# Kernel tuning notes

Measured on AMD Instinct MI355X. Metric: run time of the kernel, lower is better.

The kernel has to match this reference:

```python
import jax, jax.numpy as jnp
import numpy as np

N_NODES = 50000
N_EDGES = 800000
IN_FEAT = 64
HIDDEN = 32
GRID = 4
OUT = 1
N_GRAPHS = 128
N_CONV = 2  # num_layers - 1
NEG_SLOPE = 0.01  # torch LeakyReLU default


def kan_apply(x, W, bias=None):
    # x: (B, in), W: (2, out, in, grid) -> (B, out)
    g = W.shape[-1]
    k = jnp.arange(1, g + 1, dtype=x.dtype)          # (grid,)
    arg = x[:, :, None] * k                           # (B, in, grid)
    y = (jnp.einsum('big,oig->bo', jnp.cos(arg), W[0])
         + jnp.einsum('big,oig->bo', jnp.sin(arg), W[1]))
    if bias is not None:
        y = y + bias
    return y


def setup_inputs() -> dict:
    key = jax.random.key(0)
    ks = jax.random.split(key, 8)
    x = jax.random.normal(ks[0], (N_NODES, IN_FEAT), dtype=jnp.float32)
    edge_index = jax.random.randint(ks[1], (2, N_EDGES), 0, N_NODES, dtype=jnp.int64)
    batch = jnp.sort(jax.random.randint(ks[2], (N_NODES,), 0, N_GRAPHS, dtype=jnp.int64))
    W_in = jax.random.normal(ks[3], (2, HIDDEN, IN_FEAT, GRID), dtype=jnp.float32) / np.float32(np.sqrt(IN_FEAT) * np.sqrt(GRID))
    W_conv = jax.random.normal(ks[4], (N_CONV, 2, HIDDEN, HIDDEN, GRID), dtype=jnp.float32) / np.float32(np.sqrt(HIDDEN) * np.sqrt(GRID))
    W_out = jax.random.normal(ks[5], (2, OUT, HIDDEN, 1), dtype=jnp.float32) / np.float32(np.sqrt(HIDDEN) * 1.0)
    b_out = jnp.zeros((1, OUT), dtype=jnp.float32)
    return {"x": x, "edge_index": edge_index, "batch": batch,
            "W_in": W_in, "W_conv": W_conv, "W_out": W_out, "b_out": b_out}


def reference(x, edge_index, batch, W_in, W_conv, W_out, b_out):
    # input KAN projection: (N, in_feat) -> (N, hidden)
    h = kan_apply(x, W_in)
    src, dst = edge_index[0], edge_index[1]
    for l in range(N_CONV):
        # message: Fourier-KAN transform of gathered source features (E, hidden)
        m_edge = kan_apply(h[src], W_conv[l])
        # aggregate: scatter-add to destination nodes
        m = jax.ops.segment_sum(m_edge, dst, num_segments=N_NODES)
        h = jax.nn.leaky_relu(m + h, negative_slope=NEG_SLOPE)
    # mean pool per graph
    sums = jax.ops.segment_sum(h, batch, num_segments=N_GRAPHS)
    counts = jax.ops.segment_sum(jnp.ones((h.shape[0], 1), h.dtype), batch, num_segments=N_GRAPHS)
    y = sums / jnp.maximum(counts, 1.0)
    # readout: KAN_linear (grid=1, with bias) + sigmoid
    out = jax.nn.sigmoid(kan_apply(y, W_out, b_out))
    return out
```

## Files before the change

kernel.cpp:

```cpp
#include <hip/hip_runtime.h>
#include <math.h>

#define N_NODES   50000
#define N_EDGES   800000
#define IN_FEAT   64
#define HIDDEN    32
#define GRID_SZ   4
#define N_GRAPHS  128
#define NEG_SLOPE 0.01f
#define SCAN_BLOCKS 196

__global__ __launch_bounds__(256) void zero_int_kernel(int* __restrict__ p, int n) {
  const int i = blockIdx.x * 256 + threadIdx.x;
  if (i < n) p[i] = 0;
}
__global__ __launch_bounds__(256) void zero_kernel(float* __restrict__ p, int n) {
  const int i = blockIdx.x * 256 + threadIdx.x;
  if (i < n) p[i] = 0.f;
}

__global__ __launch_bounds__(256) void hist_kernel(
    const int* __restrict__ dst, int* __restrict__ deg) {
  const int e = blockIdx.x * 256 + threadIdx.x;
  if (e < N_EDGES) atomicAdd(&deg[dst[e]], 1);
}

__global__ __launch_bounds__(256) void scanA_kernel(
    const int* __restrict__ deg, int* __restrict__ bsum) {
  const int i = blockIdx.x * 256 + threadIdx.x;
  int v = (i < N_NODES) ? deg[i] : 0;
#pragma unroll
  for (int o = 32; o > 0; o >>= 1) v += __shfl_down(v, o, 64);
  __shared__ int ws[4];
  if ((threadIdx.x & 63) == 0) ws[threadIdx.x >> 6] = v;
  __syncthreads();
  if (threadIdx.x == 0) bsum[blockIdx.x] = ws[0] + ws[1] + ws[2] + ws[3];
}

__global__ __launch_bounds__(256) void scanB_kernel(
    int* __restrict__ bsum, int* __restrict__ row_ptr) {
  __shared__ int sh[256];
  const int t = threadIdx.x;
  int v = (t < SCAN_BLOCKS) ? bsum[t] : 0;
  sh[t] = v;
  __syncthreads();
  for (int o = 1; o < 256; o <<= 1) {
    const int u = (t >= o) ? sh[t - o] : 0;
    __syncthreads();
    sh[t] += u;
    __syncthreads();
  }
  bsum[t] = (t == 0) ? 0 : sh[t - 1];
  if (t == 0) row_ptr[N_NODES] = N_EDGES;
}

__global__ __launch_bounds__(256) void scanC_kernel(
    const int* __restrict__ deg, const int* __restrict__ bsum,
    int* __restrict__ row_ptr, int* __restrict__ cursor) {
  __shared__ int sh[256];
  const int t = threadIdx.x;
  const int i = blockIdx.x * 256 + t;
  const int v = (i < N_NODES) ? deg[i] : 0;
  sh[t] = v;
  __syncthreads();
  for (int o = 1; o < 256; o <<= 1) {
    const int u = (t >= o) ? sh[t - o] : 0;
    __syncthreads();
    sh[t] += u;
    __syncthreads();
  }
  if (i < N_NODES) {
    const int excl = bsum[blockIdx.x] + sh[t] - v;
    row_ptr[i] = excl;
    cursor[i] = excl;
  }
}

__global__ __launch_bounds__(256) void fill_kernel(
    const int* __restrict__ src, const int* __restrict__ dst,
    int* __restrict__ cursor, int* __restrict__ adj) {
  const int e = blockIdx.x * 256 + threadIdx.x;
  if (e < N_EDGES) {
    const int pos = atomicAdd(&cursor[dst[e]], 1);
    adj[pos] = src[e];
  }
}

__global__ __launch_bounds__(256) void gather_update_v2(
    const float* __restrict__ T, const int* __restrict__ row_ptr,
    const int* __restrict__ adj, float* __restrict__ H) {
  const int gid = blockIdx.x * 256 + threadIdx.x;
  const int n = gid >> 3;
  const int q = gid & 7;
  if (n >= N_NODES) return;
  const int lo = row_ptr[n], hi = row_ptr[n + 1];
  const float4* __restrict__ T4 = reinterpret_cast<const float4*>(T);
  float4 acc = make_float4(0.f, 0.f, 0.f, 0.f);
  for (int k = lo; k < hi; ++k) {
    const int s = adj[k];
    const float4 t = T4[s * 8 + q];
    acc.x += t.x; acc.y += t.y; acc.z += t.z; acc.w += t.w;
  }
  float4* __restrict__ H4 = reinterpret_cast<float4*>(H);
  float4 h = H4[n * 8 + q];
  h.x += acc.x; h.y += acc.y; h.z += acc.z; h.w += acc.w;
  h.x = (h.x >= 0.f) ? h.x : NEG_SLOPE * h.x;
  h.y = (h.y >= 0.f) ? h.y : NEG_SLOPE * h.y;
  h.z = (h.z >= 0.f) ? h.z : NEG_SLOPE * h.z;
  h.w = (h.w >= 0.f) ? h.w : NEG_SLOPE * h.w;
  H4[n * 8 + q] = h;
}

__global__ __launch_bounds__(256, 2) void kan_input_v9(
    const float* __restrict__ X, const float* __restrict__ W,
    float* __restrict__ H) {
  extern __shared__ float smem[];
  float4* __restrict__ w4 = reinterpret_cast<float4*>(smem);
  float* __restrict__ tg = smem + 16384;
  const int tid = threadIdx.x;
  const int n0 = blockIdx.x * 128;

  const float4* __restrict__ Wg = reinterpret_cast<const float4*>(W);
#pragma unroll
  for (int r = 0; r < 16; ++r) {
    const int idx = r * 256 + tid;
    const int part = idx >> 11;
    const int rem = idx & 2047;
    const int o = rem >> 6;
    const int i = rem & 63;
    w4[part * 2048 + o * 64 + (i ^ ((o >> 2) & 7))] = Wg[idx];
  }

  const int oq = tid & 7;
  const int grp = tid >> 3;
  const int nb = 4 * grp;

  float acc[4][4];
#pragma unroll
  for (int n = 0; n < 4; ++n)
#pragma unroll
    for (int q = 0; q < 4; ++q) acc[n][q] = 0.f;

  for (int ch = 0; ch < 8; ++ch) {
    __syncthreads();
#pragma unroll
    for (int p = 0; p < 4; ++p) {
      const int lin = p * 256 + tid;
      const int il = lin & 7;
      const int node = lin >> 3;
      const int gn = n0 + node;
      const int gs = (gn < N_NODES) ? gn : (N_NODES - 1);
      const float v = X[gs * IN_FEAT + ch * 8 + il];
      float s1, c1;
      sincosf(v, &s1, &c1);
      *reinterpret_cast<float2*>(&tg[il * 260 + node * 2]) = make_float2(c1, s1);
    }
    __syncthreads();
#pragma unroll
    for (int il = 0; il < 8; ++il) {
      const int i = ch * 8 + il;
      const float4 tA = *reinterpret_cast<const float4*>(&tg[il * 260 + nb * 2]);
      const float4 tB = *reinterpret_cast<const float4*>(&tg[il * 260 + nb * 2 + 4]);
      const float bc[4] = {tA.x, tA.z, tB.x, tB.z};
      const float bs[4] = {tA.y, tA.w, tB.y, tB.w};
      float cN[4][4], sN[4][4];
#pragma unroll
      for (int n = 0; n < 4; ++n) {
        const float c1 = bc[n], s1 = bs[n];
        const float c2 = c1*c1 - s1*s1, s2 = s1*c1 + c1*s1;
        const float c3 = c2*c1 - s2*s1, s3 = s2*c1 + c2*s1;
        const float c4 = c3*c1 - s3*s1, s4 = s3*c1 + c3*s1;
        cN[n][0]=c1; cN[n][1]=c2; cN[n][2]=c3; cN[n][3]=c4;
        sN[n][0]=s1; sN[n][1]=s2; sN[n][2]=s3; sN[n][3]=s4;
      }
      const int sl = i ^ oq;
#pragma unroll
      for (int q = 0; q < 4; ++q) {
        const float4 a = w4[(4 * oq + q) * 64 + sl];
        const float4 b = w4[2048 + (4 * oq + q) * 64 + sl];
#pragma unroll
        for (int n = 0; n < 4; ++n)
          acc[n][q] += cN[n][0]*a.x + cN[n][1]*a.y + cN[n][2]*a.z + cN[n][3]*a.w
                     + sN[n][0]*b.x + sN[n][1]*b.y + sN[n][2]*b.z + sN[n][3]*b.w;
      }
    }
  }
#pragma unroll
  for (int n = 0; n < 4; ++n) {
    const int gn = n0 + nb + n;
    if (gn < N_NODES)
      *reinterpret_cast<float4*>(&H[gn * HIDDEN + 4 * oq]) =
          make_float4(acc[n][0], acc[n][1], acc[n][2], acc[n][3]);
  }
}

__global__ __launch_bounds__(256, 2) void kan_node_v9(
    const float* __restrict__ Hin, const float* __restrict__ W,
    float* __restrict__ T) {
  extern __shared__ float smem[];
  float4* __restrict__ w4 = reinterpret_cast<float4*>(smem);
  float* __restrict__ tg = smem + 8192;
  const int tid = threadIdx.x;
  const int n0 = blockIdx.x * 128;

  const float4* __restrict__ Wg = reinterpret_cast<const float4*>(W);
#pragma unroll
  for (int r = 0; r < 8; ++r) {
    const int idx = r * 256 + tid;
    const int part = idx >> 10;
    const int rem = idx & 1023;
    const int o = rem >> 5;
    const int i = rem & 31;
    w4[part * 1024 + o * 32 + (i ^ ((o >> 2) & 7))] = Wg[idx];
  }

#pragma unroll
  for (int p = 0; p < 16; ++p) {
    const int lin = p * 256 + tid;
    const int il = lin & 31;
    const int node = lin >> 5;
    const int gn = n0 + node;
    const int gs = (gn < N_NODES) ? gn : (N_NODES - 1);
    const float v = Hin[gs * HIDDEN + il];
    float s1, c1;
    sincosf(v, &s1, &c1);
    *reinterpret_cast<float2*>(&tg[il * 260 + node * 2]) = make_float2(c1, s1);
  }
  __syncthreads();

  const int oq = tid & 7;
  const int grp = tid >> 3;
  const int nb = 4 * grp;

  float acc[4][4];
#pragma unroll
  for (int n = 0; n < 4; ++n)
#pragma unroll
    for (int q = 0; q < 4; ++q) acc[n][q] = 0.f;

#pragma unroll 4
  for (int i = 0; i < HIDDEN; ++i) {
    const float4 tA = *reinterpret_cast<const float4*>(&tg[i * 260 + nb * 2]);
    const float4 tB = *reinterpret_cast<const float4*>(&tg[i * 260 + nb * 2 + 4]);
    const float bc[4] = {tA.x, tA.z, tB.x, tB.z};
    const float bs[4] = {tA.y, tA.w, tB.y, tB.w};
    float cN[4][4], sN[4][4];
#pragma unroll
    for (int n = 0; n < 4; ++n) {
      const float c1 = bc[n], s1 = bs[n];
      const float c2 = c1*c1 - s1*s1, s2 = s1*c1 + c1*s1;
      const float c3 = c2*c1 - s2*s1, s3 = s2*c1 + c2*s1;
      const float c4 = c3*c1 - s3*s1, s4 = s3*c1 + c3*s1;
      cN[n][0]=c1; cN[n][1]=c2; cN[n][2]=c3; cN[n][3]=c4;
      sN[n][0]=s1; sN[n][1]=s2; sN[n][2]=s3; sN[n][3]=s4;
    }
    const int sl = i ^ oq;
#pragma unroll
    for (int q = 0; q < 4; ++q) {
      const float4 a = w4[(4 * oq + q) * 32 + sl];
      const float4 b = w4[1024 + (4 * oq + q) * 32 + sl];
#pragma unroll
      for (int n = 0; n < 4; ++n)
        acc[n][q] += cN[n][0]*a.x + cN[n][1]*a.y + cN[n][2]*a.z + cN[n][3]*a.w
                   + sN[n][0]*b.x + sN[n][1]*b.y + sN[n][2]*b.z + sN[n][3]*b.w;
    }
  }
#pragma unroll
  for (int n = 0; n < 4; ++n) {
    const int gn = n0 + nb + n;
    if (gn < N_NODES)
      *reinterpret_cast<float4*>(&T[gn * HIDDEN + 4 * oq]) =
          make_float4(acc[n][0], acc[n][1], acc[n][2], acc[n][3]);
  }
}

#define POOL_RANGES 512
__global__ __launch_bounds__(256) void pool_rl(
    const float* __restrict__ H, const int* __restrict__ batch,
    float* __restrict__ sums, float* __restrict__ cnt) {
  const int tid = threadIdx.x;
  const int f = tid & 31;
  const int r = blockIdx.x * 8 + (tid >> 5);
  const int PER = (N_NODES + POOL_RANGES - 1) / POOL_RANGES;
  int n = r * PER;
  const int end = (n + PER < N_NODES) ? n + PER : N_NODES;
  if (n >= end) return;
  int g = batch[n];
  float acc = 0.f, c = 0.f;
  for (; n < end; ++n) {
    const int gn = batch[n];
    if (gn != g) {
      atomicAdd(&sums[g * HIDDEN + f], acc);
      if (f == 0) atomicAdd(&cnt[g], c);
      g = gn; acc = 0.f; c = 0.f;
    }
    acc += H[n * HIDDEN + f];
    c += 1.f;
  }
  atomicAdd(&sums[g * HIDDEN + f], acc);
  if (f == 0) atomicAdd(&cnt[g], c);
}

__global__ __launch_bounds__(128) void readout_kernel(
    const float* __restrict__ sums, const float* __restrict__ cnt,
    const float* __restrict__ Wout, const float* __restrict__ bout,
    float* __restrict__ out) {
  const int g = threadIdx.x;
  if (g < N_GRAPHS) {
    const float c = fmaxf(cnt[g], 1.0f);
    float z = 0.f;
#pragma unroll
    for (int i = 0; i < HIDDEN; ++i) {
      const float y = sums[g * HIDDEN + i] / c;
      z += cosf(y) * Wout[i] + sinf(y) * Wout[HIDDEN + i];
    }
    z += bout[0];
    out[g] = 1.0f / (1.0f + expf(-z));
  }
}

extern "C" void kernel_launch(void* const* d_in, const int* in_sizes, int n_in,
                              void* d_out, int out_size, void* d_ws, size_t ws_size,
                              hipStream_t stream) {
  const float* x        = (const float*)d_in[0];
  const int*   eidx     = (const int*)d_in[1];
  const int*   batch    = (const int*)d_in[2];
  const float* W_in     = (const float*)d_in[3];
  const float* W_conv   = (const float*)d_in[4];
  const float* W_out    = (const float*)d_in[5];
  const float* b_out    = (const float*)d_in[6];
  float* out            = (float*)d_out;

  const int* src = eidx;
  const int* dst = eidx + N_EDGES;

  float* ws = (float*)d_ws;
  float* H       = ws;
  float* T       = ws + 1600000;
  int*   row_ptr = (int*)(ws + 3200000);
  int*   deg     = row_ptr + 50008;
  int*   cursor  = deg + 50048;
  int*   bsum    = cursor + 50048;
  int*   adj     = bsum + 256;
  float* SUMS    = (float*)(adj + 800000);
  float* CNT     = SUMS + 4096;

  const int kan_blocks  = (N_NODES + 127) / 128;
  const int edge_blocks = (N_EDGES + 255) / 256;
  const int gath_blocks = (N_NODES * 8 + 255) / 256;

  const size_t in_lds   = (size_t)(16384 + 8 * 260) * 4;
  const size_t conv_lds = (size_t)(8192 + 32 * 260) * 4;
  const int WCONV_STRIDE = 2 * HIDDEN * HIDDEN * GRID_SZ;

  zero_int_kernel<<<SCAN_BLOCKS, 256, 0, stream>>>(deg, N_NODES);
  hist_kernel<<<edge_blocks, 256, 0, stream>>>(dst, deg);
  scanA_kernel<<<SCAN_BLOCKS, 256, 0, stream>>>(deg, bsum);
  scanB_kernel<<<1, 256, 0, stream>>>(bsum, row_ptr);
  scanC_kernel<<<SCAN_BLOCKS, 256, 0, stream>>>(deg, bsum, row_ptr, cursor);
  fill_kernel<<<edge_blocks, 256, 0, stream>>>(src, dst, cursor, adj);

  kan_input_v9<<<kan_blocks, 256, in_lds, stream>>>(x, W_in, H);

  kan_node_v9<<<kan_blocks, 256, conv_lds, stream>>>(H, W_conv, T);
  gather_update_v2<<<gath_blocks, 256, 0, stream>>>(T, row_ptr, adj, H);

  kan_node_v9<<<kan_blocks, 256, conv_lds, stream>>>(H, W_conv + WCONV_STRIDE, T);
  gather_update_v2<<<gath_blocks, 256, 0, stream>>>(T, row_ptr, adj, H);

  zero_kernel<<<17, 256, 0, stream>>>(SUMS, N_GRAPHS * HIDDEN + N_GRAPHS);
  pool_rl<<<POOL_RANGES / 8, 256, 0, stream>>>(H, batch, SUMS, CNT);
  readout_kernel<<<1, 128, 0, stream>>>(SUMS, CNT, W_out, b_out, out);
}
```

Before: 308.3 us.

## Split KAN output columns across blocks and compute sincos in registers

The input and node KAN kernels now launch twice as many 128-thread blocks. Each block computes 16 of the 32 output features and stores only that half of the weights in static LDS. The shared cos/sin staging buffer and its per-chunk barriers are removed; each thread loads its four nodes' features as float4 from global memory and computes sincos itself. This cuts LDS footprint and synchronisation to raise occupancy, at the cost of doing the transcendental work twice, once in each column-half block.

```diff
diff --git a/kernel.cpp b/kernel.cpp
--- a/kernel.cpp
+++ b/kernel.cpp
@@ -111,62 +111,60 @@
   H4[n * 8 + q] = h;
 }
 
-__global__ __launch_bounds__(256, 2) void kan_input_v9(
+__global__ __launch_bounds__(128, 2) void kan_input_v10(
     const float* __restrict__ X, const float* __restrict__ W,
     float* __restrict__ H) {
-  extern __shared__ float smem[];
-  float4* __restrict__ w4 = reinterpret_cast<float4*>(smem);
-  float* __restrict__ tg = smem + 16384;
+  __shared__ float4 w4[2048];
   const int tid = threadIdx.x;
-  const int n0 = blockIdx.x * 128;
+  const int half = blockIdx.x & 1;
+  const int nblk = blockIdx.x >> 1;
+  const int n0 = nblk * 128;
 
   const float4* __restrict__ Wg = reinterpret_cast<const float4*>(W);
 #pragma unroll
   for (int r = 0; r < 16; ++r) {
-    const int idx = r * 256 + tid;
-    const int part = idx >> 11;
-    const int rem = idx & 2047;
-    const int o = rem >> 6;
+    const int idx = r * 128 + tid;
+    const int part = idx >> 10;
+    const int rem = idx & 1023;
+    const int o_l = rem >> 6;
     const int i = rem & 63;
-    w4[part * 2048 + o * 64 + (i ^ ((o >> 2) & 7))] = Wg[idx];
-  }
-
-  const int oq = tid & 7;
-  const int grp = tid >> 3;
+    w4[part * 1024 + o_l * 64 + (i ^ (o_l >> 2))] =
+        Wg[part * 2048 + (half * 16 + o_l) * 64 + i];
+  }
+  __syncthreads();
+
+  const int oq = tid & 3;
+  const int grp = tid >> 2;
   const int nb = 4 * grp;
 
+  int gs[4];
+#pragma unroll
+  for (int n = 0; n < 4; ++n) {
+    const int gn = n0 + nb + n;
+    gs[n] = (gn < N_NODES) ? gn : (N_NODES - 1);
+  }
+
   float acc[4][4];
 #pragma unroll
   for (int n = 0; n < 4; ++n)
 #pragma unroll
     for (int q = 0; q < 4; ++q) acc[n][q] = 0.f;
 
-  for (int ch = 0; ch < 8; ++ch) {
-    __syncthreads();
-#pragma unroll
-    for (int p = 0; p < 4; ++p) {
-      const int lin = p * 256 + tid;
-      const int il = lin & 7;
-      const int node = lin >> 3;
-      const int gn = n0 + node;
-      const int gs = (gn < N_NODES) ? gn : (N_NODES - 1);
-      const float v = X[gs * IN_FEAT + ch * 8 + il];
-      float s1, c1;
-      sincosf(v, &s1, &c1);
-      *reinterpret_cast<float2*>(&tg[il * 260 + node * 2]) = make_float2(c1, s1);
-    }
-    __syncthreads();
-#pragma unroll
-    for (int il = 0; il < 8; ++il) {
-      const int i = ch * 8 + il;
-      const float4 tA = *reinterpret_cast<const float4*>(&tg[il * 260 + nb * 2]);
-      const float4 tB = *reinterpret_cast<const float4*>(&tg[il * 260 + nb * 2 + 4]);
-      const float bc[4] = {tA.x, tA.z, tB.x, tB.z};
-      const float bs[4] = {tA.y, tA.w, tB.y, tB.w};
+  for (int ci = 0; ci < 16; ++ci) {
+    float4 xv[4];
+#pragma unroll
+    for (int n = 0; n < 4; ++n)
+      xv[n] = reinterpret_cast<const float4*>(X + gs[n] * IN_FEAT)[ci];
+#pragma unroll
+    for (int j = 0; j < 4; ++j) {
+      const int i = ci * 4 + j;
       float cN[4][4], sN[4][4];
 #pragma unroll
       for (int n = 0; n < 4; ++n) {
-        const float c1 = bc[n], s1 = bs[n];
+        const float v = (j == 0) ? xv[n].x : (j == 1) ? xv[n].y :
+                        (j == 2) ? xv[n].z : xv[n].w;
+        float s1, c1;
+        sincosf(v, &s1, &c1);
         const float c2 = c1*c1 - s1*s1, s2 = s1*c1 + c1*s1;
         const float c3 = c2*c1 - s2*s1, s3 = s2*c1 + c2*s1;
         const float c4 = c3*c1 - s3*s1, s4 = s3*c1 + c3*s1;
@@ -177,7 +175,7 @@
 #pragma unroll
       for (int q = 0; q < 4; ++q) {
         const float4 a = w4[(4 * oq + q) * 64 + sl];
-        const float4 b = w4[2048 + (4 * oq + q) * 64 + sl];
+        const float4 b = w4[1024 + (4 * oq + q) * 64 + sl];
 #pragma unroll
         for (int n = 0; n < 4; ++n)
           acc[n][q] += cN[n][0]*a.x + cN[n][1]*a.y + cN[n][2]*a.z + cN[n][3]*a.w
@@ -189,87 +187,88 @@
   for (int n = 0; n < 4; ++n) {
     const int gn = n0 + nb + n;
     if (gn < N_NODES)
-      *reinterpret_cast<float4*>(&H[gn * HIDDEN + 4 * oq]) =
+      *reinterpret_cast<float4*>(&H[gn * HIDDEN + half * 16 + 4 * oq]) =
           make_float4(acc[n][0], acc[n][1], acc[n][2], acc[n][3]);
   }
 }
 
-__global__ __launch_bounds__(256, 2) void kan_node_v9(
+__global__ __launch_bounds__(128, 2) void kan_node_v10(
     const float* __restrict__ Hin, const float* __restrict__ W,
     float* __restrict__ T) {
-  extern __shared__ float smem[];
-  float4* __restrict__ w4 = reinterpret_cast<float4*>(smem);
-  float* __restrict__ tg = smem + 8192;
+  __shared__ float4 w4[1024];
   const int tid = threadIdx.x;
-  const int n0 = blockIdx.x * 128;
+  const int half = blockIdx.x & 1;
+  const int nblk = blockIdx.x >> 1;
+  const int n0 = nblk * 128;
 
   const float4* __restrict__ Wg = reinterpret_cast<const float4*>(W);
 #pragma unroll
   for (int r = 0; r < 8; ++r) {
-    const int idx = r * 256 + tid;
-    const int part = idx >> 10;
-    const int rem = idx & 1023;
-    const int o = rem >> 5;
+    const int idx = r * 128 + tid;
+    const int part = idx >> 9;
+    const int rem = idx & 511;
+    const int o_l = rem >> 5;
     const int i = rem & 31;
-    w4[part * 1024 + o * 32 + (i ^ ((o >> 2) & 7))] = Wg[idx];
-  }
-
-#pragma unroll
-  for (int p = 0; p < 16; ++p) {
-    const int lin = p * 256 + tid;
-    const int il = lin & 31;
-    const int node = lin >> 5;
-    const int gn = n0 + node;
-    const int gs = (gn < N_NODES) ? gn : (N_NODES - 1);
-    const float v = Hin[gs * HIDDEN + il];
-    float s1, c1;
-    sincosf(v, &s1, &c1);
-    *reinterpret_cast<float2*>(&tg[il * 260 + node * 2]) = make_float2(c1, s1);
-  }
-  __syncthreads();
-
-  const int oq = tid & 7;
-  const int grp = tid >> 3;
+    w4[part * 512 + o_l * 32 + (i ^ (o_l >> 2))] =
+        Wg[part * 1024 + (half * 16 + o_l) * 32 + i];
+  }
+  __syncthreads();
+
+  const int oq = tid & 3;
+  const int grp = tid >> 2;
   const int nb = 4 * grp;
 
+  int gs[4];
+#pragma unroll
+  for (int n = 0; n < 4; ++n) {
+    const int gn = n0 + nb + n;
+    gs[n] = (gn < N_NODES) ? gn : (N_NODES - 1);
+  }
+
   float acc[4][4];
 #pragma unroll
   for (int n = 0; n < 4; ++n)
 #pragma unroll
     for (int q = 0; q < 4; ++q) acc[n][q] = 0.f;
 
-#pragma unroll 4
-  for (int i = 0; i < HIDDEN; ++i) {
-    const float4 tA = *reinterpret_cast<const float4*>(&tg[i * 260 + nb * 2]);
-    const float4 tB = *reinterpret_cast<const float4*>(&tg[i * 260 + nb * 2 + 4]);
-    const float bc[4] = {tA.x, tA.z, tB.x, tB.z};
-    const float bs[4] = {tA.y, tA.w, tB.y, tB.w};
-    float cN[4][4], sN[4][4];
-#pragma unroll
-    for (int n = 0; n < 4; ++n) {
-      const float c1 = bc[n], s1 = bs[n];
-      const float c2 = c1*c1 - s1*s1, s2 = s1*c1 + c1*s1;
-      const float c3 = c2*c1 - s2*s1, s3 = s2*c1 + c2*s1;
-      const float c4 = c3*c1 - s3*s1, s4 = s3*c1 + c3*s1;
-      cN[n][0]=c1; cN[n][1]=c2; cN[n][2]=c3; cN[n][3]=c4;
-      sN[n][0]=s1; sN[n][1]=s2; sN[n][2]=s3; sN[n][3]=s4;
-    }
-    const int sl = i ^ oq;
-#pragma unroll
-    for (int q = 0; q < 4; ++q) {
-      const float4 a = w4[(4 * oq + q) * 32 + sl];
-      const float4 b = w4[1024 + (4 * oq + q) * 32 + sl];
-#pragma unroll
-      for (int n = 0; n < 4; ++n)
-        acc[n][q] += cN[n][0]*a.x + cN[n][1]*a.y + cN[n][2]*a.z + cN[n][3]*a.w
-                   + sN[n][0]*b.x + sN[n][1]*b.y + sN[n][2]*b.z + sN[n][3]*b.w;
+  for (int ci = 0; ci < 8; ++ci) {
+    float4 xv[4];
+#pragma unroll
+    for (int n = 0; n < 4; ++n)
+      xv[n] = reinterpret_cast<const float4*>(Hin + gs[n] * HIDDEN)[ci];
+#pragma unroll
+    for (int j = 0; j < 4; ++j) {
+      const int i = ci * 4 + j;
+      float cN[4][4], sN[4][4];
+#pragma unroll
+      for (int n = 0; n < 4; ++n) {
+        const float v = (j == 0) ? xv[n].x : (j == 1) ? xv[n].y :
+                        (j == 2) ? xv[n].z : xv[n].w;
+        float s1, c1;
+        sincosf(v, &s1, &c1);
+        const float c2 = c1*c1 - s1*s1, s2 = s1*c1 + c1*s1;
+        const float c3 = c2*c1 - s2*s1, s3 = s2*c1 + c2*s1;
+        const float c4 = c3*c1 - s3*s1, s4 = s3*c1 + c3*s1;
+        cN[n][0]=c1; cN[n][1]=c2; cN[n][2]=c3; cN[n][3]=c4;
+        sN[n][0]=s1; sN[n][1]=s2; sN[n][2]=s3; sN[n][3]=s4;
+      }
+      const int sl = i ^ oq;
+#pragma unroll
+      for (int q = 0; q < 4; ++q) {
+        const float4 a = w4[(4 * oq + q) * 32 + sl];
+        const float4 b = w4[512 + (4 * oq + q) * 32 + sl];
+#pragma unroll
+        for (int n = 0; n < 4; ++n)
+          acc[n][q] += cN[n][0]*a.x + cN[n][1]*a.y + cN[n][2]*a.z + cN[n][3]*a.w
+                     + sN[n][0]*b.x + sN[n][1]*b.y + sN[n][2]*b.z + sN[n][3]*b.w;
+      }
     }
   }
 #pragma unroll
   for (int n = 0; n < 4; ++n) {
     const int gn = n0 + nb + n;
     if (gn < N_NODES)
-      *reinterpret_cast<float4*>(&T[gn * HIDDEN + 4 * oq]) =
+      *reinterpret_cast<float4*>(&T[gn * HIDDEN + half * 16 + 4 * oq]) =
           make_float4(acc[n][0], acc[n][1], acc[n][2], acc[n][3]);
   }
 }
@@ -345,12 +344,10 @@
   float* SUMS    = (float*)(adj + 800000);
   float* CNT     = SUMS + 4096;
 
-  const int kan_blocks  = (N_NODES + 127) / 128;
+  const int kan_blocks  = 2 * ((N_NODES + 127) / 128);
   const int edge_blocks = (N_EDGES + 255) / 256;
   const int gath_blocks = (N_NODES * 8 + 255) / 256;
 
-  const size_t in_lds   = (size_t)(16384 + 8 * 260) * 4;
-  const size_t conv_lds = (size_t)(8192 + 32 * 260) * 4;
   const int WCONV_STRIDE = 2 * HIDDEN * HIDDEN * GRID_SZ;
 
   zero_int_kernel<<<SCAN_BLOCKS, 256, 0, stream>>>(deg, N_NODES);
@@ -360,12 +357,12 @@
   scanC_kernel<<<SCAN_BLOCKS, 256, 0, stream>>>(deg, bsum, row_ptr, cursor);
   fill_kernel<<<edge_blocks, 256, 0, stream>>>(src, dst, cursor, adj);
 
-  kan_input_v9<<<kan_blocks, 256, in_lds, stream>>>(x, W_in, H);
-
-  kan_node_v9<<<kan_blocks, 256, conv_lds, stream>>>(H, W_conv, T);
+  kan_input_v10<<<kan_blocks, 128, 0, stream>>>(x, W_in, H);
+
+  kan_node_v10<<<kan_blocks, 128, 0, stream>>>(H, W_conv, T);
   gather_update_v2<<<gath_blocks, 256, 0, stream>>>(T, row_ptr, adj, H);
 
-  kan_node_v9<<<kan_blocks, 256, conv_lds, stream>>>(H, W_conv + WCONV_STRIDE, T);
+  kan_node_v10<<<kan_blocks, 128, 0, stream>>>(H, W_conv + WCONV_STRIDE, T);
   gather_update_v2<<<gath_blocks, 256, 0, stream>>>(T, row_ptr, adj, H);
 
   zero_kernel<<<17, 256, 0, stream>>>(SUMS, N_GRAPHS * HIDDEN + N_GRAPHS);
```

Result: slower. 341.2 us (+10.7%).

## Split KAN kernels by output half, unroll gather, fold zeroing into scan

Applied to the files above, without the earlier changes.

The input and conv KAN kernels now use 128-thread blocks, each computing half of the 32 output features for 128 nodes, which doubles the block count and halves the per-block weight LDS. This aims to improve occupancy and the spread of work across CUs, at the cost of recomputing the sincos/transcendental terms twice per node. The gather loop is unrolled by two to keep more independent loads in flight. The pooling buffer zeroing is folded into scanB to drop a launch, and the number of pooling ranges is raised to add parallelism in the pool step.

```diff
diff --git a/kernel.cpp b/kernel.cpp
--- a/kernel.cpp
+++ b/kernel.cpp
@@ -14,10 +14,6 @@
   const int i = blockIdx.x * 256 + threadIdx.x;
   if (i < n) p[i] = 0;
 }
-__global__ __launch_bounds__(256) void zero_kernel(float* __restrict__ p, int n) {
-  const int i = blockIdx.x * 256 + threadIdx.x;
-  if (i < n) p[i] = 0.f;
-}
 
 __global__ __launch_bounds__(256) void hist_kernel(
     const int* __restrict__ dst, int* __restrict__ deg) {
@@ -38,7 +34,8 @@
 }
 
 __global__ __launch_bounds__(256) void scanB_kernel(
-    int* __restrict__ bsum, int* __restrict__ row_ptr) {
+    int* __restrict__ bsum, int* __restrict__ row_ptr,
+    float* __restrict__ sums_zero, int nz) {
   __shared__ int sh[256];
   const int t = threadIdx.x;
   int v = (t < SCAN_BLOCKS) ? bsum[t] : 0;
@@ -52,6 +49,7 @@
   }
   bsum[t] = (t == 0) ? 0 : sh[t - 1];
   if (t == 0) row_ptr[N_NODES] = N_EDGES;
+  for (int i = t; i < nz; i += 256) sums_zero[i] = 0.f;
 }
 
 __global__ __launch_bounds__(256) void scanC_kernel(
@@ -86,7 +84,7 @@
   }
 }
 
-__global__ __launch_bounds__(256) void gather_update_v2(
+__global__ __launch_bounds__(256) void gather_update_v3(
     const float* __restrict__ T, const int* __restrict__ row_ptr,
     const int* __restrict__ adj, float* __restrict__ H) {
   const int gid = blockIdx.x * 256 + threadIdx.x;
@@ -96,9 +94,17 @@
   const int lo = row_ptr[n], hi = row_ptr[n + 1];
   const float4* __restrict__ T4 = reinterpret_cast<const float4*>(T);
   float4 acc = make_float4(0.f, 0.f, 0.f, 0.f);
-  for (int k = lo; k < hi; ++k) {
-    const int s = adj[k];
-    const float4 t = T4[s * 8 + q];
+  int k = lo;
+  for (; k + 1 < hi; k += 2) {
+    const int s0 = adj[k];
+    const int s1 = adj[k + 1];
+    const float4 t0 = T4[s0 * 8 + q];
+    const float4 t1 = T4[s1 * 8 + q];
+    acc.x += t0.x + t1.x; acc.y += t0.y + t1.y;
+    acc.z += t0.z + t1.z; acc.w += t0.w + t1.w;
+  }
+  if (k < hi) {
+    const float4 t = T4[adj[k] * 8 + q];
     acc.x += t.x; acc.y += t.y; acc.z += t.z; acc.w += t.w;
   }
   float4* __restrict__ H4 = reinterpret_cast<float4*>(H);
@@ -111,28 +117,30 @@
   H4[n * 8 + q] = h;
 }
 
-__global__ __launch_bounds__(256, 2) void kan_input_v9(
+__global__ __launch_bounds__(128, 2) void kan_input_v11(
     const float* __restrict__ X, const float* __restrict__ W,
     float* __restrict__ H) {
   extern __shared__ float smem[];
   float4* __restrict__ w4 = reinterpret_cast<float4*>(smem);
-  float* __restrict__ tg = smem + 16384;
+  float* __restrict__ tg = smem + 8192;
   const int tid = threadIdx.x;
-  const int n0 = blockIdx.x * 128;
+  const int half = blockIdx.x & 1;
+  const int n0 = (blockIdx.x >> 1) * 128;
 
   const float4* __restrict__ Wg = reinterpret_cast<const float4*>(W);
 #pragma unroll
   for (int r = 0; r < 16; ++r) {
-    const int idx = r * 256 + tid;
-    const int part = idx >> 11;
-    const int rem = idx & 2047;
-    const int o = rem >> 6;
+    const int idx = r * 128 + tid;
+    const int part = idx >> 10;
+    const int rem = idx & 1023;
+    const int o_l = rem >> 6;
     const int i = rem & 63;
-    w4[part * 2048 + o * 64 + (i ^ ((o >> 2) & 7))] = Wg[idx];
-  }
-
-  const int oq = tid & 7;
-  const int grp = tid >> 3;
+    w4[part * 1024 + o_l * 64 + (i ^ (o_l >> 2))] =
+        Wg[part * 2048 + (half * 16 + o_l) * 64 + i];
+  }
+
+  const int oq = tid & 3;
+  const int grp = tid >> 2;
   const int nb = 4 * grp;
 
   float acc[4][4];
@@ -144,8 +152,8 @@
   for (int ch = 0; ch < 8; ++ch) {
     __syncthreads();
 #pragma unroll
-    for (int p = 0; p < 4; ++p) {
-      const int lin = p * 256 + tid;
+    for (int p = 0; p < 8; ++p) {
+      const int lin = p * 128 + tid;
       const int il = lin & 7;
       const int node = lin >> 3;
       const int gn = n0 + node;
@@ -177,7 +185,7 @@
 #pragma unroll
       for (int q = 0; q < 4; ++q) {
         const float4 a = w4[(4 * oq + q) * 64 + sl];
-        const float4 b = w4[2048 + (4 * oq + q) * 64 + sl];
+        const float4 b = w4[1024 + (4 * oq + q) * 64 + sl];
 #pragma unroll
         for (int n = 0; n < 4; ++n)
           acc[n][q] += cN[n][0]*a.x + cN[n][1]*a.y + cN[n][2]*a.z + cN[n][3]*a.w
@@ -189,34 +197,36 @@
   for (int n = 0; n < 4; ++n) {
     const int gn = n0 + nb + n;
     if (gn < N_NODES)
-      *reinterpret_cast<float4*>(&H[gn * HIDDEN + 4 * oq]) =
+      *reinterpret_cast<float4*>(&H[gn * HIDDEN + half * 16 + 4 * oq]) =
           make_float4(acc[n][0], acc[n][1], acc[n][2], acc[n][3]);
   }
 }
 
-__global__ __launch_bounds__(256, 2) void kan_node_v9(
+__global__ __launch_bounds__(128, 2) void kan_node_v11(
     const float* __restrict__ Hin, const float* __restrict__ W,
     float* __restrict__ T) {
   extern __shared__ float smem[];
   float4* __restrict__ w4 = reinterpret_cast<float4*>(smem);
-  float* __restrict__ tg = smem + 8192;
+  float* __restrict__ tg = smem + 4096;
   const int tid = threadIdx.x;
-  const int n0 = blockIdx.x * 128;
+  const int half = blockIdx.x & 1;
+  const int n0 = (blockIdx.x >> 1) * 128;
 
   const float4* __restrict__ Wg = reinterpret_cast<const float4*>(W);
 #pragma unroll
   for (int r = 0; r < 8; ++r) {
-    const int idx = r * 256 + tid;
-    const int part = idx >> 10;
-    const int rem = idx & 1023;
-    const int o = rem >> 5;
+    const int idx = r * 128 + tid;
+    const int part = idx >> 9;
+    const int rem = idx & 511;
+    const int o_l = rem >> 5;
     const int i = rem & 31;
-    w4[part * 1024 + o * 32 + (i ^ ((o >> 2) & 7))] = Wg[idx];
-  }
-
-#pragma unroll
-  for (int p = 0; p < 16; ++p) {
-    const int lin = p * 256 + tid;
+    w4[part * 512 + o_l * 32 + (i ^ (o_l >> 2))] =
+        Wg[part * 1024 + (half * 16 + o_l) * 32 + i];
+  }
+
+#pragma unroll
+  for (int p = 0; p < 32; ++p) {
+    const int lin = p * 128 + tid;
     const int il = lin & 31;
     const int node = lin >> 5;
     const int gn = n0 + node;
@@ -228,8 +238,8 @@
   }
   __syncthreads();
 
-  const int oq = tid & 7;
-  const int grp = tid >> 3;
+  const int oq = tid & 3;
+  const int grp = tid >> 2;
   const int nb = 4 * grp;
 
   float acc[4][4];
@@ -258,7 +268,7 @@
 #pragma unroll
     for (int q = 0; q < 4; ++q) {
       const float4 a = w4[(4 * oq + q) * 32 + sl];
-      const float4 b = w4[1024 + (4 * oq + q) * 32 + sl];
+      const float4 b = w4[512 + (4 * oq + q) * 32 + sl];
 #pragma unroll
       for (int n = 0; n < 4; ++n)
         acc[n][q] += cN[n][0]*a.x + cN[n][1]*a.y + cN[n][2]*a.z + cN[n][3]*a.w
@@ -269,12 +279,12 @@
   for (int n = 0; n < 4; ++n) {
     const int gn = n0 + nb + n;
     if (gn < N_NODES)
-      *reinterpret_cast<float4*>(&T[gn * HIDDEN + 4 * oq]) =
+      *reinterpret_cast<float4*>(&T[gn * HIDDEN + half * 16 + 4 * oq]) =
           make_float4(acc[n][0], acc[n][1], acc[n][2], acc[n][3]);
   }
 }
 
-#define POOL_RANGES 512
+#define POOL_RANGES 2048
 __global__ __launch_bounds__(256) void pool_rl(
     const float* __restrict__ H, const int* __restrict__ batch,
     float* __restrict__ sums, float* __restrict__ cnt) {
@@ -345,30 +355,29 @@
   float* SUMS    = (float*)(adj + 800000);
   float* CNT     = SUMS + 4096;
 
-  const int kan_blocks  = (N_NODES + 127) / 128;
+  const int kan_blocks  = 2 * ((N_NODES + 127) / 128);
   const int edge_blocks = (N_EDGES + 255) / 256;
   const int gath_blocks = (N_NODES * 8 + 255) / 256;
 
-  const size_t in_lds   = (size_t)(16384 + 8 * 260) * 4;
-  const size_t conv_lds = (size_t)(8192 + 32 * 260) * 4;
+  const size_t in_lds   = (size_t)(8192 + 8 * 260) * 4;
+  const size_t conv_lds = (size_t)(4096 + 32 * 260) * 4;
   const int WCONV_STRIDE = 2 * HIDDEN * HIDDEN * GRID_SZ;
 
   zero_int_kernel<<<SCAN_BLOCKS, 256, 0, stream>>>(deg, N_NODES);
   hist_kernel<<<edge_blocks, 256, 0, stream>>>(dst, deg);
   scanA_kernel<<<SCAN_BLOCKS, 256, 0, stream>>>(deg, bsum);
-  scanB_kernel<<<1, 256, 0, stream>>>(bsum, row_ptr);
+  scanB_kernel<<<1, 256, 0, stream>>>(bsum, row_ptr, SUMS, N_GRAPHS * HIDDEN + N_GRAPHS);
   scanC_kernel<<<SCAN_BLOCKS, 256, 0, stream>>>(deg, bsum, row_ptr, cursor);
   fill_kernel<<<edge_blocks, 256, 0, stream>>>(src, dst, cursor, adj);
 
-  kan_input_v9<<<kan_blocks, 256, in_lds, stream>>>(x, W_in, H);
-
-  kan_node_v9<<<kan_blocks, 256, conv_lds, stream>>>(H, W_conv, T);
-  gather_update_v2<<<gath_blocks, 256, 0, stream>>>(T, row_ptr, adj, H);
-
-  kan_node_v9<<<kan_blocks, 256, conv_lds, stream>>>(H, W_conv + WCONV_STRIDE, T);
-  gather_update_v2<<<gath_blocks, 256, 0, stream>>>(T, row_ptr, adj, H);
-
-  zero_kernel<<<17, 256, 0, stream>>>(SUMS, N_GRAPHS * HIDDEN + N_GRAPHS);
+  kan_input_v11<<<kan_blocks, 128, in_lds, stream>>>(x, W_in, H);
+
+  kan_node_v11<<<kan_blocks, 128, conv_lds, stream>>>(H, W_conv, T);
+  gather_update_v3<<<gath_blocks, 256, 0, stream>>>(T, row_ptr, adj, H);
+
+  kan_node_v11<<<kan_blocks, 128, conv_lds, stream>>>(H, W_conv + WCONV_STRIDE, T);
+  gather_update_v3<<<gath_blocks, 256, 0, stream>>>(T, row_ptr, adj, H);
+
   pool_rl<<<POOL_RANGES / 8, 256, 0, stream>>>(H, batch, SUMS, CNT);
   readout_kernel<<<1, 128, 0, stream>>>(SUMS, CNT, W_out, b_out, out);
 }
```

Result: slower. 346.5 us (+12.4%).
